# Optimization experiments

Measured on AMD Instinct MI355X. Metric: run time of the kernel, lower is better.

The kernel has to match this reference:

```python
import jax, jax.numpy as jnp
import numpy as np

N_NODES = 100000
N_EDGES = 3200000
N_GRAPHS = 256
FEAT = 128
HIDDEN = 128
N_CLASSES = 10


def setup_inputs() -> dict:
    key = jax.random.key(0)
    ks = jax.random.split(key, 12)
    x = jax.random.normal(ks[0], (N_NODES, FEAT), dtype=jnp.float32)
    edge_index = jax.random.randint(ks[1], (2, N_EDGES), 0, N_NODES, dtype=jnp.int64)
    batch = jnp.sort(jax.random.randint(ks[2], (N_NODES,), 0, N_GRAPHS, dtype=jnp.int64))
    s = 0.05
    return {
        "x": x,
        "edge_index": edge_index,
        "batch": batch,
        "W1": jax.random.normal(ks[3], (FEAT, HIDDEN), dtype=jnp.float32) * s,
        "b1": jnp.zeros((HIDDEN,), dtype=jnp.float32),
        "W2": jax.random.normal(ks[4], (HIDDEN, HIDDEN), dtype=jnp.float32) * s,
        "b2": jnp.zeros((HIDDEN,), dtype=jnp.float32),
        "W3": jax.random.normal(ks[5], (HIDDEN, HIDDEN), dtype=jnp.float32) * s,
        "b3": jnp.zeros((HIDDEN,), dtype=jnp.float32),
        "lin1_w": jax.random.normal(ks[6], (HIDDEN, HIDDEN), dtype=jnp.float32) * s,
        "lin1_b": jnp.zeros((HIDDEN,), dtype=jnp.float32),
        "lin2_w": jax.random.normal(ks[7], (HIDDEN, N_CLASSES), dtype=jnp.float32) * s,
        "lin2_b": jnp.zeros((N_CLASSES,), dtype=jnp.float32),
    }


def _gcn_norm(edge_index, n_nodes):
    # PyG GCNConv default: add self-loops, symmetric normalization.
    src = jnp.concatenate([edge_index[0], jnp.arange(n_nodes, dtype=edge_index.dtype)])
    dst = jnp.concatenate([edge_index[1], jnp.arange(n_nodes, dtype=edge_index.dtype)])
    deg = jax.ops.segment_sum(jnp.ones_like(dst, dtype=jnp.float32), dst, num_segments=n_nodes)
    dis = jnp.where(deg > 0, jax.lax.rsqrt(jnp.maximum(deg, 1.0)), 0.0)
    norm = dis[src] * dis[dst]  # [E + N]
    return src, dst, norm


def _gcn_conv(x, src, dst, norm, W, b, n_nodes):
    h = x @ W                               # [N, H]
    msg = h[src] * norm[:, None]            # gather + scale, [E+N, H]
    out = jax.ops.segment_sum(msg, dst, num_segments=n_nodes)  # scatter-add
    return out + b


def reference(x, edge_index, batch, W1, b1, W2, b2, W3, b3, lin1_w, lin1_b, lin2_w, lin2_b):
    n = x.shape[0]
    src, dst, norm = _gcn_norm(edge_index, n)
    h = jax.nn.relu(_gcn_conv(x, src, dst, norm, W1, b1, n))
    h = jax.nn.relu(_gcn_conv(h, src, dst, norm, W2, b2, n))
    h = jax.nn.relu(_gcn_conv(h, src, dst, norm, W3, b3, n))
    # global mean pool over graphs
    sums = jax.ops.segment_sum(h, batch, num_segments=N_GRAPHS)
    cnts = jax.ops.segment_sum(jnp.ones((n,), dtype=h.dtype), batch, num_segments=N_GRAPHS)
    g = sums / jnp.maximum(cnts, 1.0)[:, None]
    g = jax.nn.relu(g @ lin1_w + lin1_b)
    # dropout p=0.5 is identity at inference
    return g @ lin2_w + lin2_b
```

## Files before the change

### kernel.cpp

```cpp
#include <hip/hip_runtime.h>
#include <hip/hip_fp16.h>

#define FEAT 128
#define CHUNK 8192
#define BSH 7
#define CAP 6144
#define RSTRIDE 784

#define QS  16.0f
#define QSI 0.0625f

typedef _Float16 half8 __attribute__((ext_vector_type(8)));
typedef float floatx4 __attribute__((ext_vector_type(4)));
typedef float floatx2 __attribute__((ext_vector_type(2)));

__device__ __forceinline__ unsigned int enc8x4(float a, float b, float c, float d) {
  unsigned int r = __builtin_amdgcn_cvt_pk_fp8_f32(a, b, 0u, false);
  return __builtin_amdgcn_cvt_pk_fp8_f32(c, d, r, true);
}
__device__ __forceinline__ void acc8(unsigned int w, float* a) {
  floatx2 v0 = __builtin_amdgcn_cvt_pk_f32_fp8(w, false);
  floatx2 v1 = __builtin_amdgcn_cvt_pk_f32_fp8(w, true);
  a[0] += v0.x; a[1] += v0.y; a[2] += v1.x; a[3] += v1.y;
}


__global__ __launch_bounds__(256) void sort_prep_kernel(
    const int* __restrict__ ei, int E, int nchunks, int nbuk,
    int* __restrict__ pairs, int* __restrict__ runs,
    const float* __restrict__ W1, const float* __restrict__ W2,
    const float* __restrict__ W3, _Float16* __restrict__ P1,
    _Float16* __restrict__ P2, _Float16* __restrict__ P3,
    unsigned char* __restrict__ qA, unsigned char* __restrict__ qB,
    float* __restrict__ gsum, int G, int N) {
  __shared__ int lhist[1024];
  __shared__ int lofs[1024];
  __shared__ int lcur[1024];
  __shared__ int tsum[256];
  __shared__ int stage[CHUNK];
  int t = threadIdx.x;
  if ((int)blockIdx.x >= nchunks) {
    int b = blockIdx.x - nchunks;
    if (b == 24) {
      if (t < 16) ((unsigned long long*)(qA + (size_t)N * FEAT))[t] = 0ull;
      else if (t < 32) ((unsigned long long*)(qB + (size_t)N * FEAT))[t - 16] = 0ull;
      return;
    }
    if (b == 25) {
      float4 z = {0.f, 0.f, 0.f, 0.f};
      for (int i = t; i < G * 32; i += 256) ((float4*)gsum)[i] = z;
      return;
    }
    const float* W = (b < 8) ? W1 : (b < 16) ? W2 : W3;
    _Float16* P = (b < 8) ? P1 : (b < 16) ? P2 : P3;
    int e = (b & 7) * 256 + t;
    int l = e & 63;
    int ks = (e >> 6) & 3;
    int tn = e >> 8;
    int n = tn * 16 + (l & 15);
    int k0 = ks * 32 + (l >> 4) * 8;
    half8 v;
#pragma unroll
    for (int j = 0; j < 8; ++j) v[j] = (_Float16)W[(k0 + j) * 128 + n];
    *(half8*)(P + (size_t)e * 8) = v;
    return;
  }
  int c = blockIdx.x;
  int e0 = c * CHUNK;
  int e1 = e0 + CHUNK; if (e1 > E) e1 = E;
  int cnt = e1 - e0;
#pragma unroll
  for (int u = 0; u < 4; ++u) lhist[t + u * 256] = 0;
  __syncthreads();
  for (int j = e0 + t; j < e1; j += 256) atomicAdd(&lhist[ei[E + j] >> BSH], 1);
  __syncthreads();
  int a0 = lhist[4 * t], a1 = lhist[4 * t + 1];
  int a2 = lhist[4 * t + 2], a3 = lhist[4 * t + 3];
  int s = ((a0 + a1) + (a2 + a3));
  tsum[t] = s;
  __syncthreads();
  for (int o = 1; o < 256; o <<= 1) {
    int x = (t >= o) ? tsum[t - o] : 0;
    __syncthreads();
    tsum[t] += x;
    __syncthreads();
  }
  int base = tsum[t] - s;
  lofs[4 * t] = base;       lcur[4 * t] = base;
  lofs[4 * t + 1] = base + a0;           lcur[4 * t + 1] = base + a0;
  lofs[4 * t + 2] = base + a0 + a1;      lcur[4 * t + 2] = base + a0 + a1;
  lofs[4 * t + 3] = base + a0 + a1 + a2; lcur[4 * t + 3] = base + a0 + a1 + a2;
  __syncthreads();
  for (int k = t; k < nbuk; k += 256) runs[(size_t)c * RSTRIDE + k] = lofs[k];
  if (t == 0) runs[(size_t)c * RSTRIDE + nbuk] = cnt;
  for (int j = e0 + t; j < e1; j += 256) {
    int sv = ei[j];
    int d = ei[E + j];
    int p = atomicAdd(&lcur[d >> BSH], 1);
    stage[p] = sv | ((d & 127) << 24);
  }
  __syncthreads();
  for (int j = t; j < cnt; j += 256) pairs[e0 + j] = stage[j];
}

__global__ __launch_bounds__(256) void csr_mm1_kernel(
    const int* __restrict__ pairs, const int* __restrict__ runs, int nchunks,
    int nbuk, int2* __restrict__ row_se, float* __restrict__ dis,
    int* __restrict__ col,
    const float* __restrict__ Av, const _Float16* __restrict__ Wpk,
    unsigned char* __restrict__ qA, int N) {
  __shared__ int rs[512], rl[512], ro[512];
  __shared__ int cnt[128], sc[128];
  __shared__ int stage[CAP];
  int t = threadIdx.x;
  if ((int)blockIdx.x >= nbuk) {
    int wave = t >> 6, lane = t & 63;
    int quad = lane >> 4, nidx = lane & 15;
    int m0 = (blockIdx.x - nbuk) * 64 + wave * 16;
    int arow = m0 + nidx;
    bool avalid = arow < N;
    floatx4 acc[8];
#pragma unroll
    for (int tn = 0; tn < 8; ++tn) acc[tn] = (floatx4){0.f, 0.f, 0.f, 0.f};
#pragma unroll
    for (int ks = 0; ks < 4; ++ks) {
      half8 x = {};
      if (avalid) {
        const float* p = Av + (size_t)arow * 128 + ks * 32 + quad * 8;
        float4 f0 = *(const float4*)p;
        float4 f1 = *(const float4*)(p + 4);
        x[0] = (_Float16)f0.x; x[1] = (_Float16)f0.y;
        x[2] = (_Float16)f0.z; x[3] = (_Float16)f0.w;
        x[4] = (_Float16)f1.x; x[5] = (_Float16)f1.y;
        x[6] = (_Float16)f1.z; x[7] = (_Float16)f1.w;
      }
#pragma unroll
      for (int tn = 0; tn < 8; ++tn) {
        half8 wfrag = *(const half8*)(Wpk + ((size_t)((tn * 4 + ks) * 64 + lane)) * 8);
        acc[tn] = __builtin_amdgcn_mfma_f32_16x16x32_f16(wfrag, x, acc[tn], 0, 0, 0);
      }
    }
    if (avalid) {
      float s = dis[arow] * QS;
#pragma unroll
      for (int tn = 0; tn < 8; ++tn) {
        unsigned int r = enc8x4(acc[tn][0] * s, acc[tn][1] * s,
                                acc[tn][2] * s, acc[tn][3] * s);
        *(unsigned int*)(qA + (size_t)arow * 128 + tn * 16 + quad * 4) = r;
      }
    }
    return;
  }
  int b = blockIdx.x;
  for (int c = t; c < 512; c += 256) {
    int s0 = 0, len = 0;
    if (c < nchunks) {
      const int* rr = runs + (size_t)c * RSTRIDE;
      s0 = rr[b];
      len = rr[b + 1] - s0;
    }
    rs[c] = s0; rl[c] = len;
  }
  if (t < 128) cnt[t] = 0;
  __syncthreads();
  ro[t] = rl[t]; ro[t + 256] = rl[t + 256];
  __syncthreads();
  for (int o = 1; o < 512; o <<= 1) {
    int v0 = (t >= o) ? ro[t - o] : 0;
    int v1 = (t + 256 >= o) ? ro[t + 256 - o] : 0;
    __syncthreads();
    ro[t] += v0; ro[t + 256] += v1;
    __syncthreads();
  }
  int ce = ro[511];
  int y0 = ro[t] - rl[t];
  int y1 = ro[t + 256] - rl[t + 256];
  __syncthreads();
  ro[t] = y0; ro[t + 256] = y1;
  __syncthreads();
  int colbase = b * CAP;
  bool fits = ce <= CAP;
  if (fits) {
    for (int c = t; c < nchunks; c += 256) {
      int gs = c * CHUNK + rs[c];
      int base = ro[c];
      int len = rl[c];
      for (int j = 0; j < len; ++j) {
        int p = pairs[gs + j];
        stage[base + j] = p;
        atomicAdd(&cnt[((unsigned)p) >> 24], 1);
      }
    }
  } else {
    for (int c = t; c < nchunks; c += 256) {
      int gs = c * CHUNK + rs[c];
      for (int j = 0; j < rl[c]; ++j)
        atomicAdd(&cnt[((unsigned)pairs[gs + j]) >> 24], 1);
    }
  }
  __syncthreads();
  int v = 0, excl = 0;
  if (t < 128) { v = cnt[t]; sc[t] = v; }
  __syncthreads();
  for (int o = 1; o < 128; o <<= 1) {
    int x = (t >= o && t < 128) ? sc[t - o] : 0;
    __syncthreads();
    if (t < 128) sc[t] += x;
    __syncthreads();
  }
  if (t < 128) {
    excl = sc[t] - v;
    int node = b * 128 + t;
    if (node < N) {
      row_se[node] = make_int2(colbase + excl, colbase + excl + v);
      dis[node] = rsqrtf((float)(v + 1));
    }
    cnt[t] = excl;
  }
  __syncthreads();
  if (fits) {
    for (int j = t; j < ce; j += 256) {
      int p = stage[j];
      int loc = atomicAdd(&cnt[((unsigned)p) >> 24], 1);
      col[colbase + loc] = (p & 0xFFFFFF) << 7;
    }
  } else {
    for (int c = t; c < nchunks; c += 256) {
      int gs = c * CHUNK + rs[c];
      for (int j = 0; j < rl[c]; ++j) {
        int p = pairs[gs + j];
        int loc = atomicAdd(&cnt[((unsigned)p) >> 24], 1);
        if (loc < CAP) col[colbase + loc] = (p & 0xFFFFFF) << 7;
      }
    }
  }
}


__global__ __launch_bounds__(256) void dis_kernel(
    const int* __restrict__ runs, int nchunks, int nbuk,
    float* __restrict__ dis, int N) {
  int node = blockIdx.x * 256 + threadIdx.x;
  if (node >= N) return;
  int b = node >> 7, sl = node & 127;
  int deg = 0;
  for (int c = 0; c < nchunks; ++c) {
    const int* rr = runs + (size_t)c * RSTRIDE;
    deg += rr[sl + 1] ? 0 : 0;
  }
  (void)b; (void)deg;
}


__global__ __launch_bounds__(256) void agg_fuse_kernel(
    const unsigned char* __restrict__ hs_in, const int2* __restrict__ row_se,
    const int* __restrict__ col, const float* __restrict__ dis,
    const float* __restrict__ bias, const _Float16* __restrict__ Wpk,
    unsigned char* __restrict__ hs_out, int N) {
  __shared__ _Float16 Xs[32][136];
  int t = threadIdx.x;
  int wave = t >> 6, lane = t & 63;
  int lin = lane & 7;
  int nl = wave * 8 + (lane >> 3);
  int node = blockIdx.x * 32 + nl;
  bool valid = node < N;
  int lin16 = lin * 16;
  int zoff = N << 7;
  float a[16];
#pragma unroll
  for (int j = 0; j < 16; ++j) a[j] = 0.f;
  int selfoff = (valid ? (node << 7) : zoff) + lin16;
  uint4 s0 = *(const uint4*)(hs_in + (unsigned)selfoff);
  acc8(s0.x, a); acc8(s0.y, a + 4); acc8(s0.z, a + 8); acc8(s0.w, a + 12);
  int2 se = valid ? row_se[node] : make_int2(0, 0);
  int i = se.x, e = se.y;
  while (__any(i < e)) {
    int c[8];
#pragma unroll
    for (int u = 0; u < 8; ++u) {
      int idx = i + u;
      c[u] = (idx < e) ? col[idx] : zoff;
    }
    uint4 r[8];
#pragma unroll
    for (int u = 0; u < 8; ++u)
      r[u] = *(const uint4*)(hs_in + (unsigned)(c[u] + lin16));
#pragma unroll
    for (int u = 0; u < 8; ++u) {
      acc8(r[u].x, a);     acc8(r[u].y, a + 4);
      acc8(r[u].z, a + 8); acc8(r[u].w, a + 12);
    }
    i += 8;
  }
  float d = valid ? dis[node] * QSI : 0.f;
  const float* bp = bias + lin16;
  half8 hx0, hx1;
#pragma unroll
  for (int j = 0; j < 8; ++j) {
    float o0 = valid ? fmaxf(fmaf(d, a[j], bp[j]), 0.f) : 0.f;
    float o1 = valid ? fmaxf(fmaf(d, a[j + 8], bp[j + 8]), 0.f) : 0.f;
    hx0[j] = (_Float16)o0;
    hx1[j] = (_Float16)o1;
  }
  *(half8*)&Xs[nl][lin16] = hx0;
  *(half8*)&Xs[nl][lin16 + 8] = hx1;
  __syncthreads();
  int quad = lane >> 4, nidx = lane & 15;
  int ntile = wave >> 1;
  int f0 = (wave & 1) * 4;
  floatx4 acc[4];
#pragma unroll
  for (int f = 0; f < 4; ++f) acc[f] = (floatx4){0.f, 0.f, 0.f, 0.f};
#pragma unroll
  for (int ks = 0; ks < 4; ++ks) {
    half8 x = *(const half8*)&Xs[ntile * 16 + nidx][ks * 32 + quad * 8];
#pragma unroll
    for (int f = 0; f < 4; ++f) {
      half8 wf = *(const half8*)(Wpk + ((size_t)(((f0 + f) * 4 + ks) * 64 + lane)) * 8);
      acc[f] = __builtin_amdgcn_mfma_f32_16x16x32_f16(wf, x, acc[f], 0, 0, 0);
    }
  }
  int onode = blockIdx.x * 32 + ntile * 16 + nidx;
  if (onode < N) {
    float sc = dis[onode] * QS;
#pragma unroll
    for (int f = 0; f < 4; ++f) {
      unsigned int rq = enc8x4(acc[f][0] * sc, acc[f][1] * sc,
                               acc[f][2] * sc, acc[f][3] * sc);
      *(unsigned int*)(hs_out + (size_t)onode * 128 + (f0 + f) * 16 + quad * 4) = rq;
    }
  }
}

__global__ __launch_bounds__(256) void agg_pool_kernel(
    const unsigned char* __restrict__ hs, const int2* __restrict__ row_se,
    const int* __restrict__ col, const float* __restrict__ dis,
    const float* __restrict__ bias, const int* __restrict__ batch,
    float* __restrict__ gsum, int N) {
  __shared__ float Hs[32][132];
  __shared__ int ig[32];
  int t = threadIdx.x;
  int wave = t >> 6, lane = t & 63;
  int lin = lane & 7;
  int nl = wave * 8 + (lane >> 3);
  int node = blockIdx.x * 32 + nl;
  bool valid = node < N;
  int lin16 = lin * 16;
  int zoff = N << 7;
  float a[16];
#pragma unroll
  for (int j = 0; j < 16; ++j) a[j] = 0.f;
  int selfoff = (valid ? (node << 7) : zoff) + lin16;
  uint4 s0 = *(const uint4*)(hs + (unsigned)selfoff);
  acc8(s0.x, a); acc8(s0.y, a + 4); acc8(s0.z, a + 8); acc8(s0.w, a + 12);
  int2 se = valid ? row_se[node] : make_int2(0, 0);
  int i = se.x, e = se.y;
  while (__any(i < e)) {
    int c[8];
#pragma unroll
    for (int u = 0; u < 8; ++u) {
      int idx = i + u;
      c[u] = (idx < e) ? col[idx] : zoff;
    }
    uint4 r[8];
#pragma unroll
    for (int u = 0; u < 8; ++u)
      r[u] = *(const uint4*)(hs + (unsigned)(c[u] + lin16));
#pragma unroll
    for (int u = 0; u < 8; ++u) {
      acc8(r[u].x, a);     acc8(r[u].y, a + 4);
      acc8(r[u].z, a + 8); acc8(r[u].w, a + 12);
    }
    i += 8;
  }
  float d = valid ? dis[node] * QSI : 0.f;
  const float* bp = bias + lin16;
#pragma unroll
  for (int j = 0; j < 16; ++j)
    Hs[nl][lin16 + j] = valid ? fmaxf(fmaf(d, a[j], bp[j]), 0.f) : 0.f;
  if (lin == 0) ig[nl] = batch[valid ? node : (N - 1)];
  __syncthreads();
  if (t < 128) {
    float run = 0.f;
    int cur = ig[0];
#pragma unroll 4
    for (int n = 0; n < 32; ++n) {
      int g2 = ig[n];
      if (g2 != cur) {
        atomicAdd(&gsum[cur * 128 + t], run);
        run = 0.f;
        cur = g2;
      }
      run += Hs[n][t];
    }
    atomicAdd(&gsum[cur * 128 + t], run);
  }
}

__global__ __launch_bounds__(128) void head_kernel(
    const float* __restrict__ gsum, const int* __restrict__ batch,
    const float* __restrict__ l1w, const float* __restrict__ l1b,
    const float* __restrict__ l2w, const float* __restrict__ l2b,
    float* __restrict__ out, int N, int C) {
  __shared__ float row[128];
  __shared__ float row2[128];
  int grp = blockIdx.x, t = threadIdx.x;
  int lo = 0, hi = N;
  while (lo < hi) { int m = (lo + hi) >> 1; if (batch[m] < grp) lo = m + 1; else hi = m; }
  int start = lo;
  hi = N;
  while (lo < hi) { int m = (lo + hi) >> 1; if (batch[m] <= grp) lo = m + 1; else hi = m; }
  int end = lo;
  float cntf = (float)(end - start);
  row[t] = gsum[grp * 128 + t] / fmaxf(cntf, 1.0f);
  __syncthreads();
  float acc = l1b[t];
#pragma unroll 8
  for (int k = 0; k < 128; ++k) acc = fmaf(row[k], l1w[k * 128 + t], acc);
  row2[t] = fmaxf(acc, 0.f);
  __syncthreads();
  if (t < C) {
    float a = l2b[t];
#pragma unroll 8
    for (int k = 0; k < 128; ++k) a = fmaf(row2[k], l2w[k * C + t], a);
    out[grp * C + t] = a;
  }
}


extern "C" void kernel_launch(void* const* d_in, const int* in_sizes, int n_in,
                              void* d_out, int out_size, void* d_ws, size_t ws_size,
                              hipStream_t stream) {
  const float* x   = (const float*)d_in[0];
  const int*   ei  = (const int*)d_in[1];
  const int*   bat = (const int*)d_in[2];
  const float* W1  = (const float*)d_in[3];
  const float* b1  = (const float*)d_in[4];
  const float* W2  = (const float*)d_in[5];
  const float* b2  = (const float*)d_in[6];
  const float* W3  = (const float*)d_in[7];
  const float* b3  = (const float*)d_in[8];
  const float* l1w = (const float*)d_in[9];
  const float* l1b = (const float*)d_in[10];
  const float* l2w = (const float*)d_in[11];
  const float* l2b = (const float*)d_in[12];

  int N = in_sizes[2];
  int E = in_sizes[1] / 2;
  int C = in_sizes[12];
  int G = out_size / C;
  float* outp = (float*)d_out;

  char* wp = (char*)d_ws;
  auto alloc = [&](size_t bytes) -> void* {
    void* p = (void*)wp;
    wp += (bytes + 255) & ~(size_t)255;
    return p;
  };
  int nbuk    = (N + 127) / 128;
  int nchunks = (E + CHUNK - 1) / CHUNK;

  float*    dis    = (float*)alloc((size_t)N * 4);
  int2*     row_se = (int2*)alloc((size_t)N * 8);
  int*      col    = (int*)alloc((size_t)nbuk * CAP * 4);
  int*      pairs  = (int*)alloc((size_t)nchunks * CHUNK * 4);
  int*      runs   = (int*)alloc((size_t)nchunks * RSTRIDE * 4);
  _Float16* Wpk1   = (_Float16*)alloc(16384 * 2);
  _Float16* Wpk2   = (_Float16*)alloc(16384 * 2);
  _Float16* Wpk3   = (_Float16*)alloc(16384 * 2);
  unsigned char* qX = (unsigned char*)alloc((size_t)(N + 1) * FEAT);
  unsigned char* qA = (unsigned char*)alloc((size_t)(N + 1) * FEAT);
  unsigned char* qB = (unsigned char*)alloc((size_t)(N + 1) * FEAT);
  float*    gsum   = (float*)alloc((size_t)G * FEAT * 4);

  sort_prep_kernel<<<nchunks + 26, 256, 0, stream>>>(
      ei, E, nchunks, nbuk, pairs, runs, W1, W2, W3, Wpk1, Wpk2, Wpk3,
      qA, qB, gsum, G, N);
  csr_mm1_kernel<<<nbuk, 256, 0, stream>>>(pairs, runs, nchunks, nbuk,
                                           row_se, dis, col,
                                           x, Wpk1, qA, N);
  csr_mm1_kernel<<<(N + 63) / 64, 256, 0, stream>>>(pairs, runs, nchunks, 0,
                                                    row_se, dis, col,
                                                    x, Wpk1, qA, N);

  int gB  = (N + 31) / 32;

  agg_fuse_kernel<<<gB, 256, 0, stream>>>(qA, row_se, col, dis, b1,
                                          Wpk2, qB, N);
  agg_fuse_kernel<<<gB, 256, 0, stream>>>(qB, row_se, col, dis, b2,
                                          Wpk3, qA, N);
  agg_pool_kernel<<<gB, 256, 0, stream>>>(qA, row_se, col, dis, b3, bat,
                                          gsum, N);
  head_kernel<<<G, 128, 0, stream>>>(gsum, bat, l1w, l1b, l2w, l2b, outp, N, C);
}
```

Before: 443.1 us.

## Merge CSR build with first matmul and apply source norm in first aggregation

The first X·W1 projection no longer scales rows by the source degree norm. That lets it run in the same launch as CSR construction instead of waiting for dis. A new first-layer aggregation kernel multiplies each gathered neighbor row by dis[src] using an extra per-edge dis lookup, with a padded dis[N] entry for invalid slots. This removes one kernel launch and the dependency barrier between CSR building and the matmul. In exchange it adds an extra random load and FMA per edge in layer 1, and it relies on the combined grid ordering so the matmul blocks do not read dis.

```diff
diff --git a/kernel.cpp b/kernel.cpp
--- a/kernel.cpp
+++ b/kernel.cpp
@@ -22,6 +22,12 @@
   floatx2 v0 = __builtin_amdgcn_cvt_pk_f32_fp8(w, false);
   floatx2 v1 = __builtin_amdgcn_cvt_pk_f32_fp8(w, true);
   a[0] += v0.x; a[1] += v0.y; a[2] += v1.x; a[3] += v1.y;
+}
+__device__ __forceinline__ void acc8s(unsigned int w, float s, float* a) {
+  floatx2 v0 = __builtin_amdgcn_cvt_pk_f32_fp8(w, false);
+  floatx2 v1 = __builtin_amdgcn_cvt_pk_f32_fp8(w, true);
+  a[0] = fmaf(s, v0.x, a[0]); a[1] = fmaf(s, v0.y, a[1]);
+  a[2] = fmaf(s, v1.x, a[2]); a[3] = fmaf(s, v1.y, a[3]);
 }
 
 
@@ -32,7 +38,7 @@
     const float* __restrict__ W3, _Float16* __restrict__ P1,
     _Float16* __restrict__ P2, _Float16* __restrict__ P3,
     unsigned char* __restrict__ qA, unsigned char* __restrict__ qB,
-    float* __restrict__ gsum, int G, int N) {
+    float* __restrict__ dis, float* __restrict__ gsum, int G, int N) {
   __shared__ int lhist[1024];
   __shared__ int lofs[1024];
   __shared__ int lcur[1024];
@@ -44,6 +50,7 @@
     if (b == 24) {
       if (t < 16) ((unsigned long long*)(qA + (size_t)N * FEAT))[t] = 0ull;
       else if (t < 32) ((unsigned long long*)(qB + (size_t)N * FEAT))[t - 16] = 0ull;
+      else if (t == 32) dis[N] = 0.f;
       return;
     }
     if (b == 25) {
@@ -141,11 +148,10 @@
       }
     }
     if (avalid) {
-      float s = dis[arow] * QS;
 #pragma unroll
       for (int tn = 0; tn < 8; ++tn) {
-        unsigned int r = enc8x4(acc[tn][0] * s, acc[tn][1] * s,
-                                acc[tn][2] * s, acc[tn][3] * s);
+        unsigned int r = enc8x4(acc[tn][0] * QS, acc[tn][1] * QS,
+                                acc[tn][2] * QS, acc[tn][3] * QS);
         *(unsigned int*)(qA + (size_t)arow * 128 + tn * 16 + quad * 4) = r;
       }
     }
@@ -237,20 +243,90 @@
 }
 
 
-__global__ __launch_bounds__(256) void dis_kernel(
-    const int* __restrict__ runs, int nchunks, int nbuk,
-    float* __restrict__ dis, int N) {
-  int node = blockIdx.x * 256 + threadIdx.x;
-  if (node >= N) return;
-  int b = node >> 7, sl = node & 127;
-  int deg = 0;
-  for (int c = 0; c < nchunks; ++c) {
-    const int* rr = runs + (size_t)c * RSTRIDE;
-    deg += rr[sl + 1] ? 0 : 0;
-  }
-  (void)b; (void)deg;
-}
-
+__global__ __launch_bounds__(256) void agg_fuse1_kernel(
+    const unsigned char* __restrict__ hs_in, const int2* __restrict__ row_se,
+    const int* __restrict__ col, const float* __restrict__ dis,
+    const float* __restrict__ bias, const _Float16* __restrict__ Wpk,
+    unsigned char* __restrict__ hs_out, int N) {
+  __shared__ _Float16 Xs[32][136];
+  int t = threadIdx.x;
+  int wave = t >> 6, lane = t & 63;
+  int lin = lane & 7;
+  int nl = wave * 8 + (lane >> 3);
+  int node = blockIdx.x * 32 + nl;
+  bool valid = node < N;
+  int lin16 = lin * 16;
+  int zoff = N << 7;
+  float a[16];
+#pragma unroll
+  for (int j = 0; j < 16; ++j) a[j] = 0.f;
+  float ds = dis[valid ? node : N];
+  int selfoff = (valid ? (node << 7) : zoff) + lin16;
+  uint4 s0 = *(const uint4*)(hs_in + (unsigned)selfoff);
+  acc8s(s0.x, ds, a); acc8s(s0.y, ds, a + 4);
+  acc8s(s0.z, ds, a + 8); acc8s(s0.w, ds, a + 12);
+  int2 se = valid ? row_se[node] : make_int2(0, 0);
+  int i = se.x, e = se.y;
+  while (__any(i < e)) {
+    int c[8];
+#pragma unroll
+    for (int u = 0; u < 8; ++u) {
+      int idx = i + u;
+      c[u] = (idx < e) ? col[idx] : zoff;
+    }
+    uint4 r[8];
+#pragma unroll
+    for (int u = 0; u < 8; ++u)
+      r[u] = *(const uint4*)(hs_in + (unsigned)(c[u] + lin16));
+    float dv[8];
+#pragma unroll
+    for (int u = 0; u < 8; ++u) dv[u] = dis[(unsigned)c[u] >> 7];
+#pragma unroll
+    for (int u = 0; u < 8; ++u) {
+      acc8s(r[u].x, dv[u], a);     acc8s(r[u].y, dv[u], a + 4);
+      acc8s(r[u].z, dv[u], a + 8); acc8s(r[u].w, dv[u], a + 12);
+    }
+    i += 8;
+  }
+  float d = valid ? dis[node] * QSI : 0.f;
+  const float* bp = bias + lin16;
+  half8 hx0, hx1;
+#pragma unroll
+  for (int j = 0; j < 8; ++j) {
+    float o0 = valid ? fmaxf(fmaf(d, a[j], bp[j]), 0.f) : 0.f;
+    float o1 = valid ? fmaxf(fmaf(d, a[j + 8], bp[j + 8]), 0.f) : 0.f;
+    hx0[j] = (_Float16)o0;
+    hx1[j] = (_Float16)o1;
+  }
+  *(half8*)&Xs[nl][lin16] = hx0;
+  *(half8*)&Xs[nl][lin16 + 8] = hx1;
+  __syncthreads();
+  int quad = lane >> 4, nidx = lane & 15;
+  int ntile = wave >> 1;
+  int f0 = (wave & 1) * 4;
+  floatx4 acc[4];
+#pragma unroll
+  for (int f = 0; f < 4; ++f) acc[f] = (floatx4){0.f, 0.f, 0.f, 0.f};
+#pragma unroll
+  for (int ks = 0; ks < 4; ++ks) {
+    half8 x = *(const half8*)&Xs[ntile * 16 + nidx][ks * 32 + quad * 8];
+#pragma unroll
+    for (int f = 0; f < 4; ++f) {
+      half8 wf = *(const half8*)(Wpk + ((size_t)(((f0 + f) * 4 + ks) * 64 + lane)) * 8);
+      acc[f] = __builtin_amdgcn_mfma_f32_16x16x32_f16(wf, x, acc[f], 0, 0, 0);
+    }
+  }
+  int onode = blockIdx.x * 32 + ntile * 16 + nidx;
+  if (onode < N) {
+    float sc = dis[onode] * QS;
+#pragma unroll
+    for (int f = 0; f < 4; ++f) {
+      unsigned int rq = enc8x4(acc[f][0] * sc, acc[f][1] * sc,
+                               acc[f][2] * sc, acc[f][3] * sc);
+      *(unsigned int*)(hs_out + (size_t)onode * 128 + (f0 + f) * 16 + quad * 4) = rq;
+    }
+  }
+}
 
 __global__ __launch_bounds__(256) void agg_fuse_kernel(
     const unsigned char* __restrict__ hs_in, const int2* __restrict__ row_se,
@@ -459,8 +535,9 @@
   };
   int nbuk    = (N + 127) / 128;
   int nchunks = (E + CHUNK - 1) / CHUNK;
-
-  float*    dis    = (float*)alloc((size_t)N * 4);
+  int mmB     = (N + 63) / 64;
+
+  float*    dis    = (float*)alloc((size_t)(N + 1) * 4);
   int2*     row_se = (int2*)alloc((size_t)N * 8);
   int*      col    = (int*)alloc((size_t)nbuk * CAP * 4);
   int*      pairs  = (int*)alloc((size_t)nchunks * CHUNK * 4);
@@ -468,25 +545,20 @@
   _Float16* Wpk1   = (_Float16*)alloc(16384 * 2);
   _Float16* Wpk2   = (_Float16*)alloc(16384 * 2);
   _Float16* Wpk3   = (_Float16*)alloc(16384 * 2);
-  unsigned char* qX = (unsigned char*)alloc((size_t)(N + 1) * FEAT);
   unsigned char* qA = (unsigned char*)alloc((size_t)(N + 1) * FEAT);
   unsigned char* qB = (unsigned char*)alloc((size_t)(N + 1) * FEAT);
   float*    gsum   = (float*)alloc((size_t)G * FEAT * 4);
 
   sort_prep_kernel<<<nchunks + 26, 256, 0, stream>>>(
       ei, E, nchunks, nbuk, pairs, runs, W1, W2, W3, Wpk1, Wpk2, Wpk3,
-      qA, qB, gsum, G, N);
-  csr_mm1_kernel<<<nbuk, 256, 0, stream>>>(pairs, runs, nchunks, nbuk,
-                                           row_se, dis, col,
-                                           x, Wpk1, qA, N);
-  csr_mm1_kernel<<<(N + 63) / 64, 256, 0, stream>>>(pairs, runs, nchunks, 0,
-                                                    row_se, dis, col,
-                                                    x, Wpk1, qA, N);
-
-  int gB  = (N + 31) / 32;
-
-  agg_fuse_kernel<<<gB, 256, 0, stream>>>(qA, row_se, col, dis, b1,
-                                          Wpk2, qB, N);
+      qA, qB, dis, gsum, G, N);
+  csr_mm1_kernel<<<nbuk + mmB, 256, 0, stream>>>(pairs, runs, nchunks, nbuk,
+                                                 row_se, dis, col,
+                                                 x, Wpk1, qA, N);
+
+  int gB = (N + 31) / 32;
+  agg_fuse1_kernel<<<gB, 256, 0, stream>>>(qA, row_se, col, dis, b1,
+                                           Wpk2, qB, N);
   agg_fuse_kernel<<<gB, 256, 0, stream>>>(qB, row_se, col, dis, b2,
                                           Wpk3, qA, N);
   agg_pool_kernel<<<gB, 256, 0, stream>>>(qA, row_se, col, dis, b3, bat,
```

Result: faster. 432.5 us (-2.4%).
